# Kernel tuning notes

Hardware: AMD Instinct MI355X
Metric: run time of the kernel (lower is better)

## Reference

```python
import jax, jax.numpy as jnp
import numpy as np

HIDDEN = 384
NDIM = 3
N_POINTS = 100000
N_SUPER = 2048
MAX_DEG = 32
RADIUS = 0.045
INPUT_DIM = 3


def _sincos_embed(coords):
    # ContinuousSincosEmbed: dim=384, ndim=3 -> 128 channels per spatial dim (64 sin + 64 cos)
    eff = HIDDEN // NDIM  # 128
    omega = jnp.arange(0, eff, 2, dtype=jnp.float32) / eff
    freq = 1.0 / (10000.0 ** omega)  # [eff//2]
    out = coords[..., None] * freq  # [..., ndim, eff//2]
    emb = jnp.concatenate([jnp.sin(out), jnp.cos(out)], axis=-1)  # [..., ndim, eff]
    return emb.reshape(coords.shape[:-1] + (HIDDEN,))


def _radius_neighbors(pos, sn_idx):
    # numpy preprocessing equivalent of torch_geometric.nn.pool.radius with
    # max_num_neighbors=MAX_DEG; fixed-size padded [S, K] output + validity mask.
    nbr = np.zeros((N_SUPER, MAX_DEG), np.int32)
    mask = np.zeros((N_SUPER, MAX_DEG), bool)
    pos2 = (pos ** 2).sum(-1)
    r2 = RADIUS * RADIUS
    chunk = 128
    for i0 in range(0, N_SUPER, chunk):
        sp = pos[sn_idx[i0:i0 + chunk]]
        d2 = (sp ** 2).sum(-1)[:, None] + pos2[None, :] - 2.0 * (sp @ pos.T)
        within = d2 <= r2
        for j in range(sp.shape[0]):
            idx = np.nonzero(within[j])[0][:MAX_DEG]
            nbr[i0 + j, :len(idx)] = idx
            mask[i0 + j, :len(idx)] = True
    return nbr, mask


def setup_inputs() -> dict:
    rng = np.random.default_rng(0)
    pos = rng.random((N_POINTS, NDIM)).astype(np.float32)
    sn_idx = np.sort(rng.choice(N_POINTS, N_SUPER, replace=False)).astype(np.int32)
    nbr, mask = _radius_neighbors(pos, sn_idx)
    key = jax.random.key(0)
    ks = jax.random.split(key, 6)
    s = 0.02  # truncnormal002 init scale
    return {
        "input_pos": jnp.asarray(pos),
        "input_feat": jax.random.normal(ks[0], (N_POINTS, INPUT_DIM), jnp.float32),
        "supernode_idx": jnp.asarray(sn_idx),
        "neighbor_idx": jnp.asarray(nbr),
        "neighbor_mask": jnp.asarray(mask),
        "W_in": jax.random.normal(ks[1], (INPUT_DIM, HIDDEN), jnp.float32) * s,
        "b_in": jnp.zeros((HIDDEN,), jnp.float32),
        "W1": jax.random.normal(ks[2], (2 * HIDDEN, HIDDEN), jnp.float32) * s,
        "b1": jnp.zeros((HIDDEN,), jnp.float32),
        "W2": jax.random.normal(ks[3], (HIDDEN, HIDDEN), jnp.float32) * s,
        "b2": jnp.zeros((HIDDEN,), jnp.float32),
        "W_proj": jax.random.normal(ks[4], (2 * HIDDEN, HIDDEN), jnp.float32) * s,
        "b_proj": jnp.zeros((HIDDEN,), jnp.float32),
    }


def reference(input_pos, input_feat, supernode_idx, neighbor_idx, neighbor_mask,
              W_in, b_in, W1, b1, W2, b2, W_proj, b_proj):
    # point embeddings: continuous sincos pos embed + input feature projection
    x = _sincos_embed(input_pos) + input_feat @ W_in + b_in          # [N, D]
    sn = x[supernode_idx]                                            # [S, D] supernode pos embed
    src = x[neighbor_idx]                                            # [S, K, D] gathered neighbors
    dst = jnp.broadcast_to(sn[:, None, :], src.shape)                # [S, K, D]
    h = jnp.concatenate([src, dst], axis=-1)                         # [S, K, 2D]
    # message MLP (Linear -> GELU(exact) -> Linear), as nn.GELU default
    h = jax.nn.gelu(h @ W1 + b1, approximate=False) @ W2 + b2        # [S, K, D]
    # masked mean == segment_csr(..., reduce='mean') over variable-degree edges
    m = neighbor_mask[..., None].astype(h.dtype)
    agg = (h * m).sum(axis=1) / jnp.maximum(m.sum(axis=1), 1.0)      # [S, D]
    # readd_supernode_pos: concat supernode pos embed, project 2D -> D
    out = jnp.concatenate([agg, sn], axis=-1) @ W_proj + b_proj      # [S, D]
    return out[None]                                                 # [1, S, D] (batch_size=1)
```

## Files before the change

kernel.cpp:

```cpp
#include <hip/hip_runtime.h>
#include <hip/hip_bf16.h>
#include <cstdint>

#define HIDDEN 384
#define NSUPER 2048
#define MAXDEG 32
#define FRAGS (12*24*64)
#define WBLK  (FRAGS*8)

typedef __attribute__((ext_vector_type(8))) short bf16x8;
typedef __attribute__((ext_vector_type(4))) float f32x4;

__device__ inline unsigned short f2bf(float f) {
    unsigned int u = __float_as_uint(f);
    return (unsigned short)((u + 0x7fffu + ((u >> 16) & 1u)) >> 16);
}
__device__ inline float b2f(unsigned short s) {
    return __uint_as_float(((unsigned int)s) << 16);
}
__device__ inline bf16x8 pack8(const float* v) {
    union { bf16x8 v8; unsigned short u[8]; } u;
    #pragma unroll
    for (int i = 0; i < 8; ++i) u.u[i] = f2bf(v[i]);
    return u.v8;
}
__device__ inline float gelu(float y) {
    const float y2 = y * y;
    const float m  = __expf(y * fmaf(-0.0713548163f, y2, -1.5957691216f));
    return y * (1.0f / (1.0f + m));
}

__global__ __launch_bounds__(256)
void prep(const float* __restrict__ W1, const float* __restrict__ W2,
          const float* __restrict__ Wp, const unsigned int* __restrict__ mask,
          const float* __restrict__ pos, const float* __restrict__ feat,
          const int* __restrict__ sn_idx,
          const float* __restrict__ W_in, const float* __restrict__ b_in,
          unsigned short* __restrict__ w1sf, unsigned short* __restrict__ w1df,
          unsigned short* __restrict__ w2f,  unsigned short* __restrict__ wpf,
          unsigned short* __restrict__ snxb, int* __restrict__ flag) {
    const int b = blockIdx.x;
    const int t = threadIdx.x;
    if (b == 360) {
        __shared__ int s;
        if (t == 0) s = 0;
        __syncthreads();
        int bad = 0;
        for (int i = t; i < 16384; i += 256)
            if (mask[i] > 1u) bad = 1;
        if (bad) s = 1;
        __syncthreads();
        if (t == 0) *flag = s;
        return;
    }
    if (b > 360) {
        __shared__ float W4[HIDDEN][4];
        __shared__ float P6[64][7];
        const int eb = b - 361;
        if (t < 64) {
            const int pi = sn_idx[eb*64 + t];
            P6[t][0]=pos[pi*3];  P6[t][1]=pos[pi*3+1];  P6[t][2]=pos[pi*3+2];
            P6[t][3]=feat[pi*3]; P6[t][4]=feat[pi*3+1]; P6[t][5]=feat[pi*3+2];
        }
        for (int d = t; d < HIDDEN; d += 256) {
            W4[d][0]=W_in[d]; W4[d][1]=W_in[HIDDEN+d];
            W4[d][2]=W_in[2*HIDDEN+d]; W4[d][3]=b_in[d];
        }
        __syncthreads();
        const int er = t >> 2, seg = t & 3;
        float frA[8], frB[8];
        #pragma unroll
        for (int i = 0; i < 8; ++i) {
            frA[i] = exp2f(-(float)(seg*8 + i)      * 0.2076205059304601f);
            frB[i] = exp2f(-(float)(32 + seg*8 + i) * 0.2076205059304601f);
        }
        const float f0 = P6[er][3], f1 = P6[er][4], f2 = P6[er][5];
        #pragma unroll
        for (int cc = 0; cc < 3; ++cc) {
            const float pc = P6[er][cc];
            float sL[8], sH[8], cL[8], cH[8];
            #pragma unroll
            for (int i = 0; i < 8; ++i) {
                const float aL = pc*frA[i], aH = pc*frB[i];
                sL[i]=__sinf(aL); sH[i]=__sinf(aH); cL[i]=__cosf(aL); cH[i]=__cosf(aH);
            }
            #pragma unroll
            for (int q = 0; q < 4; ++q) {
                const float* bb = (q==0)?sL:(q==1)?sH:(q==2)?cL:cH;
                const int blk = cc*4 + q;
                float v[8];
                #pragma unroll
                for (int i = 0; i < 8; ++i) {
                    const int dim = blk*32 + seg*8 + i;
                    const float4 wv = *(const float4*)W4[dim];
                    v[i] = fmaf(f0, wv.x, fmaf(f1, wv.y, fmaf(f2, wv.z, bb[i] + wv.w)));
                }
                *(bf16x8*)&snxb[(size_t)(eb*64 + er)*HIDDEN + blk*32 + seg*8] = pack8(v);
            }
        }
        return;
    }
    const int grp = b / 72, sub = b % 72;
    const float* W; unsigned short* out;
    switch (grp) {
        case 0: W = W1;              out = w1sf; break;
        case 1: W = W1 + 384*HIDDEN; out = w1df; break;
        case 2: W = W2;              out = w2f;  break;
        case 3: W = Wp;              out = wpf;  break;
        default:W = Wp + 384*HIDDEN; out = wpf + WBLK; break;
    }
    const int idx = sub * 256 + t;
    const int l   = idx & 63;
    const int frag= idx >> 6;
    const int nt  = frag % 24;
    const int kt  = frag / 24;
    const int col = nt * 16 + (l & 15);
    const int k0  = kt * 32 + (l >> 4) * 8;
    unsigned int pk[4];
    #pragma unroll
    for (int j = 0; j < 4; ++j) {
        unsigned int lo = f2bf(W[(k0 + 2*j)     * HIDDEN + col]);
        unsigned int hi = f2bf(W[(k0 + 2*j + 1) * HIDDEN + col]);
        pk[j] = lo | (hi << 16);
    }
    *reinterpret_cast<uint4*>(&out[(size_t)idx * 8]) =
        *reinterpret_cast<const uint4*>(pk);
}

__global__ __launch_bounds__(256, 2)
void k_mlp(const float* __restrict__ pos, const float* __restrict__ feat,
           const int* __restrict__ nbr_idx, const void* __restrict__ mask_raw,
           const int* __restrict__ mask_fmt,
           const float* __restrict__ W_in, const float* __restrict__ b_in,
           const unsigned short* __restrict__ snxb,
           const unsigned short* __restrict__ W1sf,
           const unsigned short* __restrict__ W1df,
           const unsigned short* __restrict__ W2f,
           const float* __restrict__ b1, const float* __restrict__ b2,
           unsigned short* __restrict__ aggb)
{
    __shared__ unsigned short G[4*12*64*8];
    __shared__ ushort4 WINTB[HIDDEN];
    __shared__ float PF[64][7];
    __shared__ float CNT[2];

    const int t  = threadIdx.x;
    const int bm = blockIdx.x;
    const int l = t & 63, ng = t >> 6, lg = l >> 4, l15 = l & 15;

    bf16x8 bA[6], bB[6];
    #define LOADB(dst, Wf, kt)                                                  \
        { const unsigned short* bp_ = &Wf[((size_t)((kt)*24 + ng*6)*64 + l)*8]; \
          _Pragma("unroll")                                                     \
          for (int nt_ = 0; nt_ < 6; ++nt_)                                     \
              dst[nt_] = *(const bf16x8*)(bp_ + (size_t)nt_*512); }
    #define AREAD(a_, kt)                                                       \
        { _Pragma("unroll")                                                     \
          for (int mt_ = 0; mt_ < 4; ++mt_)                                     \
              a_[mt_] = *(const bf16x8*)&G[(size_t)(((mt_*12 + (kt))*64) + l)*8]; }
    #define MFMA6(bfr, a_)                                                      \
        { __builtin_amdgcn_s_setprio(1);                                        \
          _Pragma("unroll")                                                     \
          for (int mt_ = 0; mt_ < 4; ++mt_)                                     \
              _Pragma("unroll")                                                 \
              for (int nt_ = 0; nt_ < 6; ++nt_)                                 \
                  acc[mt_][nt_] = __builtin_amdgcn_mfma_f32_16x16x32_bf16(      \
                      a_[mt_], bfr[nt_], acc[mt_][nt_], 0, 0, 0);               \
          __builtin_amdgcn_s_setprio(0); }

    if (t < 64) {
        const int e  = bm*64 + t;
        const int pi = nbr_idx[e];
        PF[t][0]=pos[pi*3];  PF[t][1]=pos[pi*3+1];  PF[t][2]=pos[pi*3+2];
        PF[t][3]=feat[pi*3]; PF[t][4]=feat[pi*3+1]; PF[t][5]=feat[pi*3+2];
        const int fmt = *mask_fmt;
        const int mv  = fmt ? (int)((const unsigned char*)mask_raw)[e]
                            : ((const int*)mask_raw)[e];
        PF[t][6] = mv ? 1.0f : 0.0f;
    }
    for (int d = t; d < HIDDEN; d += 256) {
        ushort4 wv;
        wv.x = f2bf(W_in[d]); wv.y = f2bf(W_in[HIDDEN+d]);
        wv.z = f2bf(W_in[2*HIDDEN+d]); wv.w = f2bf(b_in[d]);
        WINTB[d] = wv;
    }
    float b1r[6];
    #pragma unroll
    for (int nt = 0; nt < 6; ++nt) b1r[nt] = b1[ng*96 + nt*16 + l15];
    __syncthreads();
    if (t < 2) {
        float c = 0.f;
        for (int s = 0; s < 32; ++s) c += PF[t*32+s][6];
        CNT[t] = c;
    }

    const int er = t >> 2, seg = t & 3;
    float frA[8], frB[8];
    #pragma unroll
    for (int i = 0; i < 8; ++i) {
        frA[i] = exp2f(-(float)(seg*8 + i)      * 0.2076205059304601f);
        frB[i] = exp2f(-(float)(32 + seg*8 + i) * 0.2076205059304601f);
    }
    const float f0 = PF[er][3], f1 = PF[er][4], f2 = PF[er][5];
    const float pc0 = PF[er][0], pc1 = PF[er][1], pc2 = PF[er][2];
    const int slotbase = (er>>4)*12*64 + seg*16 + (er&15);

    #define EMB(kt_)                                                            \
        { const float pc = ((kt_)>>2)==0 ? pc0 : (((kt_)>>2)==1 ? pc1 : pc2);   \
          float v[8];                                                           \
          _Pragma("unroll")                                                     \
          for (int i = 0; i < 8; ++i) {                                         \
              const float fr = ((kt_)&1) ? frB[i] : frA[i];                     \
              const float aa = pc * fr;                                         \
              const float base = (((kt_)>>1)&1) ? __cosf(aa) : __sinf(aa);      \
              const ushort4 wv = WINTB[(kt_)*32 + seg*8 + i];                   \
              v[i] = fmaf(f0, b2f(wv.x), fmaf(f1, b2f(wv.y),                    \
                     fmaf(f2, b2f(wv.z), base + b2f(wv.w))));                   \
          }                                                                     \
          *(bf16x8*)&G[(size_t)(slotbase + (kt_)*64)*8] = pack8(v); }

    f32x4 acc[4][6];
    #pragma unroll
    for (int mt=0; mt<4; ++mt)
        #pragma unroll
        for (int nt=0; nt<6; ++nt) acc[mt][nt] = (f32x4){0.f,0.f,0.f,0.f};

    const unsigned short* snx0 = &snxb[(size_t)(bm*2 + 0)*HIDDEN];
    const unsigned short* snx1 = &snxb[(size_t)(bm*2 + 1)*HIDDEN];
    #pragma unroll
    for (int kt = 0; kt < 12; ++kt) {
        LOADB(bA, W1df, kt);
        bf16x8 s0 = *(const bf16x8*)&snx0[kt*32 + lg*8];
        bf16x8 s1 = *(const bf16x8*)&snx1[kt*32 + lg*8];
        EMB(kt);
        __builtin_amdgcn_s_setprio(1);
        #pragma unroll
        for (int nt = 0; nt < 6; ++nt) {
            acc[0][nt] = __builtin_amdgcn_mfma_f32_16x16x32_bf16(s0, bA[nt], acc[0][nt], 0,0,0);
            acc[1][nt] = __builtin_amdgcn_mfma_f32_16x16x32_bf16(s0, bA[nt], acc[1][nt], 0,0,0);
            acc[2][nt] = __builtin_amdgcn_mfma_f32_16x16x32_bf16(s1, bA[nt], acc[2][nt], 0,0,0);
            acc[3][nt] = __builtin_amdgcn_mfma_f32_16x16x32_bf16(s1, bA[nt], acc[3][nt], 0,0,0);
        }
        __builtin_amdgcn_s_setprio(0);
    }
    __syncthreads();

    LOADB(bA, W1sf, 0); LOADB(bB, W1sf, 1);
    #pragma unroll
    for (int kt = 0; kt < 12; kt += 2) {
        bf16x8 a[4];
        AREAD(a, kt);
        MFMA6(bA, a);
        if (kt + 2 < 12) LOADB(bA, W1sf, kt + 2);
        AREAD(a, kt + 1);
        MFMA6(bB, a);
        if (kt + 3 < 12) LOADB(bB, W1sf, kt + 3);
    }
    __syncthreads();

    #pragma unroll
    for (int mt=0; mt<4; ++mt) {
        #pragma unroll
        for (int nt=0; nt<6; ++nt) {
            const int col = ng*96 + nt*16 + l15;
            const float bb1 = b1r[nt];
            const int base = ((mt*12 + (col>>5))*64 + ((col>>3)&3)*16 + lg*4)*8 + (col&7);
            #pragma unroll
            for (int r=0; r<4; ++r)
                G[base + r*8] = f2bf(gelu(acc[mt][nt][r] + bb1));
        }
    }
    __syncthreads();

    #pragma unroll
    for (int mt=0; mt<4; ++mt)
        #pragma unroll
        for (int nt=0; nt<6; ++nt) acc[mt][nt] = (f32x4){0.f,0.f,0.f,0.f};
    LOADB(bA, W2f, 0); LOADB(bB, W2f, 1);
    #pragma unroll
    for (int kt = 0; kt < 12; kt += 2) {
        bf16x8 a[4];
        AREAD(a, kt);
        MFMA6(bA, a);
        if (kt + 2 < 12) LOADB(bA, W2f, kt + 2);
        AREAD(a, kt + 1);
        MFMA6(bB, a);
        if (kt + 3 < 12) LOADB(bB, W2f, kt + 3);
    }

    #pragma unroll
    for (int nt=0; nt<6; ++nt) {
        const int col = ng*96 + nt*16 + l15;
        float s0 = 0.f, s1 = 0.f;
        #pragma unroll
        for (int mt=0; mt<4; ++mt) {
            float p = 0.f;
            #pragma unroll
            for (int r=0; r<4; ++r)
                p += PF[mt*16 + lg*4 + r][6] * acc[mt][nt][r];
            if (mt < 2) s0 += p; else s1 += p;
        }
        s0 += __shfl_xor(s0,16); s0 += __shfl_xor(s0,32);
        s1 += __shfl_xor(s1,16); s1 += __shfl_xor(s1,32);
        if (lg == 0) {
            const float bb = b2[col];
            const int sn0 = bm*2;
            const float c0 = CNT[0], c1 = CNT[1];
            aggb[(size_t)sn0*HIDDEN + col]     = f2bf(s0 / fmaxf(c0,1.f) + bb*(c0>0.f?1.f:0.f));
            aggb[(size_t)(sn0+1)*HIDDEN + col] = f2bf(s1 / fmaxf(c1,1.f) + bb*(c1>0.f?1.f:0.f));
        }
    }
    #undef LOADB
    #undef AREAD
    #undef MFMA6
    #undef EMB
}

__global__ __launch_bounds__(256)
void k_proj(const unsigned short* __restrict__ aggb,
            const unsigned short* __restrict__ snxb,
            const unsigned short* __restrict__ wpf,
            const float* __restrict__ bp, float* __restrict__ out) {
    const int rg = blockIdx.x >> 2, cq = blockIdx.x & 3;
    const int t = threadIdx.x, w = t>>6, l = t&63, lg = l>>4, l15 = l&15;
    const int wgm = w>>1, wgn = w&1;
    const int r0 = rg*64 + wgm*32;
    const int ntb = cq*6 + wgn*3;
    f32x4 acc[2][3];
    #pragma unroll
    for (int mt=0; mt<2; ++mt)
        #pragma unroll
        for (int nt=0; nt<3; ++nt) acc[mt][nt] = (f32x4){0.f,0.f,0.f,0.f};
    #pragma unroll 2
    for (int kt = 0; kt < 24; ++kt) {
        const unsigned short* Ab = (kt < 12) ? aggb : snxb;
        const unsigned short* Wb = (kt < 12) ? wpf  : wpf + WBLK;
        const int ktt = (kt < 12) ? kt : kt - 12;
        bf16x8 a[2], bfr[3];
        const unsigned short* bpp = &Wb[((size_t)(ktt*24 + ntb)*64 + l)*8];
        #pragma unroll
        for (int nt=0; nt<3; ++nt) bfr[nt] = *(const bf16x8*)(bpp + (size_t)nt*512);
        #pragma unroll
        for (int mt=0; mt<2; ++mt)
            a[mt] = *(const bf16x8*)&Ab[(size_t)(r0 + mt*16 + l15)*HIDDEN + ktt*32 + lg*8];
        #pragma unroll
        for (int mt=0; mt<2; ++mt)
            #pragma unroll
            for (int nt=0; nt<3; ++nt)
                acc[mt][nt] = __builtin_amdgcn_mfma_f32_16x16x32_bf16(a[mt], bfr[nt], acc[mt][nt], 0,0,0);
    }
    #pragma unroll
    for (int mt=0; mt<2; ++mt)
        #pragma unroll
        for (int nt=0; nt<3; ++nt) {
            const int col = cq*96 + wgn*48 + nt*16 + l15;
            #pragma unroll
            for (int r=0; r<4; ++r) {
                const int row = r0 + mt*16 + lg*4 + r;
                out[(size_t)row*HIDDEN + col] = acc[mt][nt][r] + bp[col];
            }
        }
}

extern "C" void kernel_launch(void* const* d_in, const int* in_sizes, int n_in,
                              void* d_out, int out_size, void* d_ws, size_t ws_size,
                              hipStream_t stream) {
    const float* pos   = (const float*)d_in[0];
    const float* feat  = (const float*)d_in[1];
    const int*   sn    = (const int*)d_in[2];
    const int*   nbr   = (const int*)d_in[3];
    const void*  mask  = d_in[4];
    const float* W_in  = (const float*)d_in[5];
    const float* b_in  = (const float*)d_in[6];
    const float* W1    = (const float*)d_in[7];
    const float* b1    = (const float*)d_in[8];
    const float* W2    = (const float*)d_in[9];
    const float* b2    = (const float*)d_in[10];
    const float* Wp    = (const float*)d_in[11];
    const float* bpv   = (const float*)d_in[12];
    float* out = (float*)d_out;

    char* base = (char*)d_ws;
    int* flag = (int*)base;
    unsigned short* w1sf = (unsigned short*)(base + 256);
    unsigned short* w1df = w1sf + WBLK;
    unsigned short* w2f  = w1df + WBLK;
    unsigned short* wpf  = w2f  + WBLK;
    unsigned short* snxb = wpf  + 2*(size_t)WBLK;
    unsigned short* aggb = snxb + (size_t)NSUPER*HIDDEN;

    hipLaunchKernelGGL(prep, dim3(393), dim3(256), 0, stream,
                       W1, W2, Wp, (const unsigned int*)mask,
                       pos, feat, sn, W_in, b_in,
                       w1sf, w1df, w2f, wpf, snxb, flag);
    hipLaunchKernelGGL(k_mlp, dim3(1024), dim3(256), 0, stream,
                       pos, feat, nbr, mask, flag, W_in, b_in,
                       snxb, w1sf, w1df, w2f, b1, b2, aggb);
    hipLaunchKernelGGL(k_proj, dim3(128), dim3(256), 0, stream,
                       aggb, snxb, wpf, bpv, out);
}
```

Baseline: 84.44 us.

## Move second MLP linear after masked mean aggregation into separate GEMM kernel

The second linear layer is linear, so the masked mean of its output equals the masked mean of the GELU activations multiplied by W2, plus the bias when the node has neighbors. k_mlp now only computes GEMM1 plus GELU and reduces over neighbors, writing pre-aggregated bf16 rows and counts. A new k_agg kernel applies W2 and the bias on the 2048 supernode rows. This removes the per-edge W2 GEMM and the LDS staging of activations, at the cost of an extra launch and an extra workspace buffer.

```diff
diff --git a/kernel.cpp b/kernel.cpp
--- a/kernel.cpp
+++ b/kernel.cpp
@@ -135,9 +135,8 @@
            const unsigned short* __restrict__ snxb,
            const unsigned short* __restrict__ W1sf,
            const unsigned short* __restrict__ W1df,
-           const unsigned short* __restrict__ W2f,
-           const float* __restrict__ b1, const float* __restrict__ b2,
-           unsigned short* __restrict__ aggb)
+           const float* __restrict__ b1,
+           unsigned short* __restrict__ aggpre, float* __restrict__ cntf)
 {
     __shared__ unsigned short G[4*12*64*8];
     __shared__ ushort4 WINTB[HIDDEN];
@@ -256,64 +255,78 @@
         MFMA6(bB, a);
         if (kt + 3 < 12) LOADB(bB, W1sf, kt + 3);
     }
-    __syncthreads();
-
-    #pragma unroll
-    for (int mt=0; mt<4; ++mt) {
-        #pragma unroll
-        for (int nt=0; nt<6; ++nt) {
-            const int col = ng*96 + nt*16 + l15;
-            const float bb1 = b1r[nt];
-            const int base = ((mt*12 + (col>>5))*64 + ((col>>3)&3)*16 + lg*4)*8 + (col&7);
-            #pragma unroll
-            for (int r=0; r<4; ++r)
-                G[base + r*8] = f2bf(gelu(acc[mt][nt][r] + bb1));
-        }
-    }
-    __syncthreads();
-
-    #pragma unroll
-    for (int mt=0; mt<4; ++mt)
-        #pragma unroll
-        for (int nt=0; nt<6; ++nt) acc[mt][nt] = (f32x4){0.f,0.f,0.f,0.f};
-    LOADB(bA, W2f, 0); LOADB(bB, W2f, 1);
-    #pragma unroll
-    for (int kt = 0; kt < 12; kt += 2) {
-        bf16x8 a[4];
-        AREAD(a, kt);
-        MFMA6(bA, a);
-        if (kt + 2 < 12) LOADB(bA, W2f, kt + 2);
-        AREAD(a, kt + 1);
-        MFMA6(bB, a);
-        if (kt + 3 < 12) LOADB(bB, W2f, kt + 3);
-    }
 
     #pragma unroll
     for (int nt=0; nt<6; ++nt) {
         const int col = ng*96 + nt*16 + l15;
+        const float bb1 = b1r[nt];
         float s0 = 0.f, s1 = 0.f;
         #pragma unroll
         for (int mt=0; mt<4; ++mt) {
             float p = 0.f;
             #pragma unroll
             for (int r=0; r<4; ++r)
-                p += PF[mt*16 + lg*4 + r][6] * acc[mt][nt][r];
+                p += PF[mt*16 + lg*4 + r][6] * gelu(acc[mt][nt][r] + bb1);
             if (mt < 2) s0 += p; else s1 += p;
         }
         s0 += __shfl_xor(s0,16); s0 += __shfl_xor(s0,32);
         s1 += __shfl_xor(s1,16); s1 += __shfl_xor(s1,32);
         if (lg == 0) {
-            const float bb = b2[col];
             const int sn0 = bm*2;
-            const float c0 = CNT[0], c1 = CNT[1];
-            aggb[(size_t)sn0*HIDDEN + col]     = f2bf(s0 / fmaxf(c0,1.f) + bb*(c0>0.f?1.f:0.f));
-            aggb[(size_t)(sn0+1)*HIDDEN + col] = f2bf(s1 / fmaxf(c1,1.f) + bb*(c1>0.f?1.f:0.f));
-        }
-    }
+            aggpre[(size_t)sn0*HIDDEN + col]     = f2bf(s0 / fmaxf(CNT[0],1.f));
+            aggpre[(size_t)(sn0+1)*HIDDEN + col] = f2bf(s1 / fmaxf(CNT[1],1.f));
+        }
+    }
+    if (t < 2) cntf[bm*2 + t] = CNT[t];
     #undef LOADB
     #undef AREAD
     #undef MFMA6
     #undef EMB
+}
+
+__global__ __launch_bounds__(256)
+void k_agg(const unsigned short* __restrict__ aggpre,
+           const unsigned short* __restrict__ w2f,
+           const float* __restrict__ b2, const float* __restrict__ cntf,
+           unsigned short* __restrict__ aggb) {
+    const int rg = blockIdx.x >> 2, cq = blockIdx.x & 3;
+    const int t = threadIdx.x, w = t>>6, l = t&63, lg = l>>4, l15 = l&15;
+    const int wgm = w>>1, wgn = w&1;
+    const int r0 = rg*64 + wgm*32;
+    const int ntb = cq*6 + wgn*3;
+    f32x4 acc[2][3];
+    #pragma unroll
+    for (int mt=0; mt<2; ++mt)
+        #pragma unroll
+        for (int nt=0; nt<3; ++nt) acc[mt][nt] = (f32x4){0.f,0.f,0.f,0.f};
+    #pragma unroll 2
+    for (int kt = 0; kt < 12; ++kt) {
+        bf16x8 a[2], bfr[3];
+        const unsigned short* bpp = &w2f[((size_t)(kt*24 + ntb)*64 + l)*8];
+        #pragma unroll
+        for (int nt=0; nt<3; ++nt) bfr[nt] = *(const bf16x8*)(bpp + (size_t)nt*512);
+        #pragma unroll
+        for (int mt=0; mt<2; ++mt)
+            a[mt] = *(const bf16x8*)&aggpre[(size_t)(r0 + mt*16 + l15)*HIDDEN + kt*32 + lg*8];
+        #pragma unroll
+        for (int mt=0; mt<2; ++mt)
+            #pragma unroll
+            for (int nt=0; nt<3; ++nt)
+                acc[mt][nt] = __builtin_amdgcn_mfma_f32_16x16x32_bf16(a[mt], bfr[nt], acc[mt][nt], 0,0,0);
+    }
+    #pragma unroll
+    for (int mt=0; mt<2; ++mt)
+        #pragma unroll
+        for (int nt=0; nt<3; ++nt) {
+            const int col = cq*96 + wgn*48 + nt*16 + l15;
+            const float bb = b2[col];
+            #pragma unroll
+            for (int r=0; r<4; ++r) {
+                const int row = r0 + mt*16 + lg*4 + r;
+                const float nz = (cntf[row] > 0.f) ? 1.f : 0.f;
+                aggb[(size_t)row*HIDDEN + col] = f2bf(acc[mt][nt][r] + bb*nz);
+            }
+        }
 }
 
 __global__ __launch_bounds__(256)
@@ -388,6 +401,8 @@
     unsigned short* wpf  = w2f  + WBLK;
     unsigned short* snxb = wpf  + 2*(size_t)WBLK;
     unsigned short* aggb = snxb + (size_t)NSUPER*HIDDEN;
+    unsigned short* aggp = aggb + (size_t)NSUPER*HIDDEN;
+    float* cntf = (float*)(aggp + (size_t)NSUPER*HIDDEN);
 
     hipLaunchKernelGGL(prep, dim3(393), dim3(256), 0, stream,
                        W1, W2, Wp, (const unsigned int*)mask,
@@ -395,7 +410,9 @@
                        w1sf, w1df, w2f, wpf, snxb, flag);
     hipLaunchKernelGGL(k_mlp, dim3(1024), dim3(256), 0, stream,
                        pos, feat, nbr, mask, flag, W_in, b_in,
-                       snxb, w1sf, w1df, w2f, b1, b2, aggb);
+                       snxb, w1sf, w1df, b1, aggp, cntf);
+    hipLaunchKernelGGL(k_agg, dim3(128), dim3(256), 0, stream,
+                       aggp, w2f, b2, cntf, aggb);
     hipLaunchKernelGGL(k_proj, dim3(128), dim3(256), 0, stream,
                        aggb, snxb, wpf, bpv, out);
 }
```

Measured after the change: 81.17 us. -3.9%, faster.

## Fold W2 into projection via linearity and split embedding into separate kernel

Applied to the files above, without the earlier changes.

Because the masked mean is linear, the second MLP layer is pushed past the aggregation: W2·Wp is precomputed in prep (fp32 matmul per fragment) and b2·Wp is added conditioned on nonzero count. This removes the whole 64x384x384 second GEMM per block in k_mlp. The neighbor embedding is moved to a separate k_emb kernel that writes MFMA-ready fragments to global workspace, chunked to fit ws_size, and k_mlp now reads A-fragments from global instead of LDS. The trade-off is a costly naive W2·Wp product in prep on every call, extra global traffic for embeddings, and a rounding change from the fused bf16 weight.

```diff
diff --git a/kernel.cpp b/kernel.cpp
--- a/kernel.cpp
+++ b/kernel.cpp
@@ -4,9 +4,9 @@
 
 #define HIDDEN 384
 #define NSUPER 2048
-#define MAXDEG 32
 #define FRAGS (12*24*64)
 #define WBLK  (FRAGS*8)
+#define EGSLOTS 3072
 
 typedef __attribute__((ext_vector_type(8))) short bf16x8;
 typedef __attribute__((ext_vector_type(4))) float f32x4;
@@ -14,9 +14,6 @@
 __device__ inline unsigned short f2bf(float f) {
     unsigned int u = __float_as_uint(f);
     return (unsigned short)((u + 0x7fffu + ((u >> 16) & 1u)) >> 16);
-}
-__device__ inline float b2f(unsigned short s) {
-    return __uint_as_float(((unsigned int)s) << 16);
 }
 __device__ inline bf16x8 pack8(const float* v) {
     union { bf16x8 v8; unsigned short u[8]; } u;
@@ -32,16 +29,18 @@
 
 __global__ __launch_bounds__(256)
 void prep(const float* __restrict__ W1, const float* __restrict__ W2,
-          const float* __restrict__ Wp, const unsigned int* __restrict__ mask,
+          const float* __restrict__ Wp, const float* __restrict__ b2,
+          const unsigned int* __restrict__ mask,
           const float* __restrict__ pos, const float* __restrict__ feat,
           const int* __restrict__ sn_idx,
           const float* __restrict__ W_in, const float* __restrict__ b_in,
           unsigned short* __restrict__ w1sf, unsigned short* __restrict__ w1df,
-          unsigned short* __restrict__ w2f,  unsigned short* __restrict__ wpf,
+          unsigned short* __restrict__ w2pf, unsigned short* __restrict__ wpbf,
+          float* __restrict__ c2p,
           unsigned short* __restrict__ snxb, int* __restrict__ flag) {
     const int b = blockIdx.x;
     const int t = threadIdx.x;
-    if (b == 360) {
+    if (b == 288) {
         __shared__ int s;
         if (t == 0) s = 0;
         __syncthreads();
@@ -53,10 +52,19 @@
         if (t == 0) *flag = s;
         return;
     }
-    if (b > 360) {
+    if (b == 289) {
+        for (int col = t; col < HIDDEN; col += 256) {
+            float s = 0.f;
+            for (int k = 0; k < HIDDEN; ++k)
+                s += b2[k] * Wp[(size_t)k*HIDDEN + col];
+            c2p[col] = s;
+        }
+        return;
+    }
+    if (b >= 290) {
         __shared__ float W4[HIDDEN][4];
         __shared__ float P6[64][7];
-        const int eb = b - 361;
+        const int eb = b - 290;
         if (t < 64) {
             const int pi = sn_idx[eb*64 + t];
             P6[t][0]=pos[pi*3];  P6[t][1]=pos[pi*3+1];  P6[t][2]=pos[pi*3+2];
@@ -100,14 +108,40 @@
         }
         return;
     }
+    if (b >= 216) {
+        const int idx = (b - 216)*256 + t;
+        const int l = idx & 63, frag = idx >> 6;
+        const int nt = frag % 24, kt = frag / 24;
+        const int col = nt*16 + (l & 15);
+        const int r0  = kt*32 + (l >> 4)*8;
+        float a8[8];
+        #pragma unroll
+        for (int j = 0; j < 8; ++j) a8[j] = 0.f;
+        for (int k = 0; k < HIDDEN; k += 4) {
+            const float wp0 = Wp[(size_t)(k+0)*HIDDEN + col];
+            const float wp1 = Wp[(size_t)(k+1)*HIDDEN + col];
+            const float wp2 = Wp[(size_t)(k+2)*HIDDEN + col];
+            const float wp3 = Wp[(size_t)(k+3)*HIDDEN + col];
+            #pragma unroll
+            for (int j = 0; j < 8; ++j) {
+                const float4 w2v = *(const float4*)&W2[(size_t)(r0+j)*HIDDEN + k];
+                a8[j] += w2v.x*wp0 + w2v.y*wp1 + w2v.z*wp2 + w2v.w*wp3;
+            }
+        }
+        unsigned int pk[4];
+        #pragma unroll
+        for (int j = 0; j < 4; ++j)
+            pk[j] = (unsigned int)f2bf(a8[2*j]) | ((unsigned int)f2bf(a8[2*j+1]) << 16);
+        *reinterpret_cast<uint4*>(&w2pf[(size_t)idx*8]) =
+            *reinterpret_cast<const uint4*>(pk);
+        return;
+    }
     const int grp = b / 72, sub = b % 72;
     const float* W; unsigned short* out;
     switch (grp) {
         case 0: W = W1;              out = w1sf; break;
         case 1: W = W1 + 384*HIDDEN; out = w1df; break;
-        case 2: W = W2;              out = w2f;  break;
-        case 3: W = Wp;              out = wpf;  break;
-        default:W = Wp + 384*HIDDEN; out = wpf + WBLK; break;
+        default:W = Wp + 384*HIDDEN; out = wpbf; break;
     }
     const int idx = sub * 256 + t;
     const int l   = idx & 63;
@@ -119,34 +153,104 @@
     unsigned int pk[4];
     #pragma unroll
     for (int j = 0; j < 4; ++j) {
-        unsigned int lo = f2bf(W[(k0 + 2*j)     * HIDDEN + col]);
-        unsigned int hi = f2bf(W[(k0 + 2*j + 1) * HIDDEN + col]);
+        unsigned int lo = f2bf(W[(size_t)(k0 + 2*j)     * HIDDEN + col]);
+        unsigned int hi = f2bf(W[(size_t)(k0 + 2*j + 1) * HIDDEN + col]);
         pk[j] = lo | (hi << 16);
     }
     *reinterpret_cast<uint4*>(&out[(size_t)idx * 8]) =
         *reinterpret_cast<const uint4*>(pk);
 }
 
+__global__ __launch_bounds__(256)
+void k_emb(const float* __restrict__ pos, const float* __restrict__ feat,
+           const int* __restrict__ nbr_idx,
+           const float* __restrict__ W_in, const float* __restrict__ b_in,
+           unsigned short* __restrict__ eG, int cbase)
+{
+    __shared__ float PF[64][6];
+    __shared__ float W4[HIDDEN][4];
+    const int t = threadIdx.x;
+    const int bmL = blockIdx.x, bmG = cbase + bmL;
+    if (t < 64) {
+        const int pi = nbr_idx[bmG*64 + t];
+        PF[t][0]=pos[pi*3];  PF[t][1]=pos[pi*3+1];  PF[t][2]=pos[pi*3+2];
+        PF[t][3]=feat[pi*3]; PF[t][4]=feat[pi*3+1]; PF[t][5]=feat[pi*3+2];
+    }
+    for (int d = t; d < HIDDEN; d += 256) {
+        W4[d][0]=W_in[d]; W4[d][1]=W_in[HIDDEN+d];
+        W4[d][2]=W_in[2*HIDDEN+d]; W4[d][3]=b_in[d];
+    }
+    __syncthreads();
+    const int er = t >> 2, seg = t & 3;
+    float frA[8], frB[8];
+    #pragma unroll
+    for (int i = 0; i < 8; ++i) {
+        frA[i] = exp2f(-(float)(seg*8 + i)      * 0.2076205059304601f);
+        frB[i] = exp2f(-(float)(32 + seg*8 + i) * 0.2076205059304601f);
+    }
+    const float f0 = PF[er][3], f1 = PF[er][4], f2 = PF[er][5];
+    const int slotb = (er>>4)*768 + seg*16 + (er&15);
+    unsigned short* dst = &eG[(size_t)bmL * EGSLOTS * 8];
+    #pragma unroll
+    for (int cc = 0; cc < 3; ++cc) {
+        const float pc = PF[er][cc];
+        float sL[8], sH[8], cL[8], cH[8];
+        #pragma unroll
+        for (int i = 0; i < 8; ++i) {
+            const float aL = pc*frA[i], aH = pc*frB[i];
+            sL[i]=__sinf(aL); sH[i]=__sinf(aH); cL[i]=__cosf(aL); cH[i]=__cosf(aH);
+        }
+        #pragma unroll
+        for (int q = 0; q < 4; ++q) {
+            const float* bb = (q==0)?sL:(q==1)?sH:(q==2)?cL:cH;
+            const int blk = cc*4 + q;
+            float v[8];
+            #pragma unroll
+            for (int i = 0; i < 8; ++i) {
+                const int dim = blk*32 + seg*8 + i;
+                const float4 wv = *(const float4*)W4[dim];
+                v[i] = fmaf(f0, wv.x, fmaf(f1, wv.y, fmaf(f2, wv.z, bb[i] + wv.w)));
+            }
+            *(bf16x8*)&dst[(size_t)(slotb + blk*64)*8] = pack8(v);
+        }
+    }
+}
+
 __global__ __launch_bounds__(256, 2)
-void k_mlp(const float* __restrict__ pos, const float* __restrict__ feat,
-           const int* __restrict__ nbr_idx, const void* __restrict__ mask_raw,
+void k_mlp(const int* __restrict__ nbr_idx, const void* __restrict__ mask_raw,
            const int* __restrict__ mask_fmt,
-           const float* __restrict__ W_in, const float* __restrict__ b_in,
            const unsigned short* __restrict__ snxb,
            const unsigned short* __restrict__ W1sf,
            const unsigned short* __restrict__ W1df,
-           const unsigned short* __restrict__ W2f,
-           const float* __restrict__ b1, const float* __restrict__ b2,
-           unsigned short* __restrict__ aggb)
+           const unsigned short* __restrict__ eG,
+           const float* __restrict__ b1,
+           unsigned short* __restrict__ aggpre, float* __restrict__ cntf,
+           int cbase)
 {
-    __shared__ unsigned short G[4*12*64*8];
-    __shared__ ushort4 WINTB[HIDDEN];
-    __shared__ float PF[64][7];
+    __shared__ float MV[64];
     __shared__ float CNT[2];
-
-    const int t  = threadIdx.x;
-    const int bm = blockIdx.x;
+    const int t = threadIdx.x;
+    const int bmL = blockIdx.x, bmG = cbase + bmL;
     const int l = t & 63, ng = t >> 6, lg = l >> 4, l15 = l & 15;
+
+    if (t < 64) {
+        const int e = bmG*64 + t;
+        const int fmt = *mask_fmt;
+        const int mv = fmt ? (int)((const unsigned char*)mask_raw)[e]
+                           : ((const int*)mask_raw)[e];
+        MV[t] = mv ? 1.0f : 0.0f;
+    }
+    __syncthreads();
+    if (t < 2) {
+        float c = 0.f;
+        for (int s = 0; s < 32; ++s) c += MV[t*32+s];
+        CNT[t] = c;
+    }
+    __syncthreads();
+
+    float b1r[6];
+    #pragma unroll
+    for (int nt = 0; nt < 6; ++nt) b1r[nt] = b1[ng*96 + nt*16 + l15];
 
     bf16x8 bA[6], bB[6];
     #define LOADB(dst, Wf, kt)                                                  \
@@ -154,10 +258,10 @@
           _Pragma("unroll")                                                     \
           for (int nt_ = 0; nt_ < 6; ++nt_)                                     \
               dst[nt_] = *(const bf16x8*)(bp_ + (size_t)nt_*512); }
-    #define AREAD(a_, kt)                                                       \
+    #define ALOAD(a_, kt)                                                       \
         { _Pragma("unroll")                                                     \
           for (int mt_ = 0; mt_ < 4; ++mt_)                                     \
-              a_[mt_] = *(const bf16x8*)&G[(size_t)(((mt_*12 + (kt))*64) + l)*8]; }
+              a_[mt_] = *(const bf16x8*)&eGb[(size_t)(((mt_*12 + (kt))*64) + l)*8]; }
     #define MFMA6(bfr, a_)                                                      \
         { __builtin_amdgcn_s_setprio(1);                                        \
           _Pragma("unroll")                                                     \
@@ -168,71 +272,24 @@
                       a_[mt_], bfr[nt_], acc[mt_][nt_], 0, 0, 0);               \
           __builtin_amdgcn_s_setprio(0); }
 
-    if (t < 64) {
-        const int e  = bm*64 + t;
-        const int pi = nbr_idx[e];
-        PF[t][0]=pos[pi*3];  PF[t][1]=pos[pi*3+1];  PF[t][2]=pos[pi*3+2];
-        PF[t][3]=feat[pi*3]; PF[t][4]=feat[pi*3+1]; PF[t][5]=feat[pi*3+2];
-        const int fmt = *mask_fmt;
-        const int mv  = fmt ? (int)((const unsigned char*)mask_raw)[e]
-                            : ((const int*)mask_raw)[e];
-        PF[t][6] = mv ? 1.0f : 0.0f;
-    }
-    for (int d = t; d < HIDDEN; d += 256) {
-        ushort4 wv;
-        wv.x = f2bf(W_in[d]); wv.y = f2bf(W_in[HIDDEN+d]);
-        wv.z = f2bf(W_in[2*HIDDEN+d]); wv.w = f2bf(b_in[d]);
-        WINTB[d] = wv;
-    }
-    float b1r[6];
-    #pragma unroll
-    for (int nt = 0; nt < 6; ++nt) b1r[nt] = b1[ng*96 + nt*16 + l15];
-    __syncthreads();
-    if (t < 2) {
-        float c = 0.f;
-        for (int s = 0; s < 32; ++s) c += PF[t*32+s][6];
-        CNT[t] = c;
-    }
-
-    const int er = t >> 2, seg = t & 3;
-    float frA[8], frB[8];
-    #pragma unroll
-    for (int i = 0; i < 8; ++i) {
-        frA[i] = exp2f(-(float)(seg*8 + i)      * 0.2076205059304601f);
-        frB[i] = exp2f(-(float)(32 + seg*8 + i) * 0.2076205059304601f);
-    }
-    const float f0 = PF[er][3], f1 = PF[er][4], f2 = PF[er][5];
-    const float pc0 = PF[er][0], pc1 = PF[er][1], pc2 = PF[er][2];
-    const int slotbase = (er>>4)*12*64 + seg*16 + (er&15);
-
-    #define EMB(kt_)                                                            \
-        { const float pc = ((kt_)>>2)==0 ? pc0 : (((kt_)>>2)==1 ? pc1 : pc2);   \
-          float v[8];                                                           \
-          _Pragma("unroll")                                                     \
-          for (int i = 0; i < 8; ++i) {                                         \
-              const float fr = ((kt_)&1) ? frB[i] : frA[i];                     \
-              const float aa = pc * fr;                                         \
-              const float base = (((kt_)>>1)&1) ? __cosf(aa) : __sinf(aa);      \
-              const ushort4 wv = WINTB[(kt_)*32 + seg*8 + i];                   \
-              v[i] = fmaf(f0, b2f(wv.x), fmaf(f1, b2f(wv.y),                    \
-                     fmaf(f2, b2f(wv.z), base + b2f(wv.w))));                   \
-          }                                                                     \
-          *(bf16x8*)&G[(size_t)(slotbase + (kt_)*64)*8] = pack8(v); }
-
     f32x4 acc[4][6];
     #pragma unroll
     for (int mt=0; mt<4; ++mt)
         #pragma unroll
         for (int nt=0; nt<6; ++nt) acc[mt][nt] = (f32x4){0.f,0.f,0.f,0.f};
 
-    const unsigned short* snx0 = &snxb[(size_t)(bm*2 + 0)*HIDDEN];
-    const unsigned short* snx1 = &snxb[(size_t)(bm*2 + 1)*HIDDEN];
+    const unsigned short* eGb = &eG[(size_t)bmL * EGSLOTS * 8];
+
+    bf16x8 aX[4], aY[4];
+    ALOAD(aX, 0);
+    ALOAD(aY, 1);
+    const unsigned short* snx0 = &snxb[(size_t)(bmG*2 + 0)*HIDDEN];
+    const unsigned short* snx1 = &snxb[(size_t)(bmG*2 + 1)*HIDDEN];
     #pragma unroll
     for (int kt = 0; kt < 12; ++kt) {
         LOADB(bA, W1df, kt);
         bf16x8 s0 = *(const bf16x8*)&snx0[kt*32 + lg*8];
         bf16x8 s1 = *(const bf16x8*)&snx1[kt*32 + lg*8];
-        EMB(kt);
         __builtin_amdgcn_s_setprio(1);
         #pragma unroll
         for (int nt = 0; nt < 6; ++nt) {
@@ -243,84 +300,57 @@
         }
         __builtin_amdgcn_s_setprio(0);
     }
-    __syncthreads();
-
-    LOADB(bA, W1sf, 0); LOADB(bB, W1sf, 1);
+
+    LOADB(bA, W1sf, 0);
+    LOADB(bB, W1sf, 1);
     #pragma unroll
     for (int kt = 0; kt < 12; kt += 2) {
-        bf16x8 a[4];
-        AREAD(a, kt);
-        MFMA6(bA, a);
-        if (kt + 2 < 12) LOADB(bA, W1sf, kt + 2);
-        AREAD(a, kt + 1);
-        MFMA6(bB, a);
-        if (kt + 3 < 12) LOADB(bB, W1sf, kt + 3);
-    }
-    __syncthreads();
-
-    #pragma unroll
-    for (int mt=0; mt<4; ++mt) {
-        #pragma unroll
-        for (int nt=0; nt<6; ++nt) {
-            const int col = ng*96 + nt*16 + l15;
-            const float bb1 = b1r[nt];
-            const int base = ((mt*12 + (col>>5))*64 + ((col>>3)&3)*16 + lg*4)*8 + (col&7);
-            #pragma unroll
-            for (int r=0; r<4; ++r)
-                G[base + r*8] = f2bf(gelu(acc[mt][nt][r] + bb1));
-        }
-    }
-    __syncthreads();
-
+        MFMA6(bA, aX);
+        if (kt + 2 < 12) { ALOAD(aX, kt + 2); LOADB(bA, W1sf, kt + 2); }
+        MFMA6(bB, aY);
+        if (kt + 3 < 12) { ALOAD(aY, kt + 3); LOADB(bB, W1sf, kt + 3); }
+    }
+
+    float mvr[4][4];
     #pragma unroll
     for (int mt=0; mt<4; ++mt)
         #pragma unroll
-        for (int nt=0; nt<6; ++nt) acc[mt][nt] = (f32x4){0.f,0.f,0.f,0.f};
-    LOADB(bA, W2f, 0); LOADB(bB, W2f, 1);
-    #pragma unroll
-    for (int kt = 0; kt < 12; kt += 2) {
-        bf16x8 a[4];
-        AREAD(a, kt);
-        MFMA6(bA, a);
-        if (kt + 2 < 12) LOADB(bA, W2f, kt + 2);
-        AREAD(a, kt + 1);
-        MFMA6(bB, a);
-        if (kt + 3 < 12) LOADB(bB, W2f, kt + 3);
-    }
-
+        for (int r=0; r<4; ++r)
+            mvr[mt][r] = MV[mt*16 + lg*4 + r];
     #pragma unroll
     for (int nt=0; nt<6; ++nt) {
         const int col = ng*96 + nt*16 + l15;
+        const float bb1 = b1r[nt];
         float s0 = 0.f, s1 = 0.f;
         #pragma unroll
         for (int mt=0; mt<4; ++mt) {
             float p = 0.f;
             #pragma unroll
             for (int r=0; r<4; ++r)
-                p += PF[mt*16 + lg*4 + r][6] * acc[mt][nt][r];
+                p += mvr[mt][r] * gelu(acc[mt][nt][r] + bb1);
             if (mt < 2) s0 += p; else s1 += p;
         }
         s0 += __shfl_xor(s0,16); s0 += __shfl_xor(s0,32);
         s1 += __shfl_xor(s1,16); s1 += __shfl_xor(s1,32);
         if (lg == 0) {
-            const float bb = b2[col];
-            const int sn0 = bm*2;
-            const float c0 = CNT[0], c1 = CNT[1];
-            aggb[(size_t)sn0*HIDDEN + col]     = f2bf(s0 / fmaxf(c0,1.f) + bb*(c0>0.f?1.f:0.f));
-            aggb[(size_t)(sn0+1)*HIDDEN + col] = f2bf(s1 / fmaxf(c1,1.f) + bb*(c1>0.f?1.f:0.f));
-        }
-    }
+            const int sn0 = bmG*2;
+            aggpre[(size_t)sn0*HIDDEN + col]     = f2bf(s0 / fmaxf(CNT[0],1.f));
+            aggpre[(size_t)(sn0+1)*HIDDEN + col] = f2bf(s1 / fmaxf(CNT[1],1.f));
+        }
+    }
+    if (t < 2) cntf[bmG*2 + t] = CNT[t];
     #undef LOADB
-    #undef AREAD
+    #undef ALOAD
     #undef MFMA6
-    #undef EMB
 }
 
 __global__ __launch_bounds__(256)
-void k_proj(const unsigned short* __restrict__ aggb,
+void k_proj(const unsigned short* __restrict__ aggp,
             const unsigned short* __restrict__ snxb,
-            const unsigned short* __restrict__ wpf,
-            const float* __restrict__ bp, float* __restrict__ out) {
+            const unsigned short* __restrict__ w2pf,
+            const unsigned short* __restrict__ wpbf,
+            const float* __restrict__ bp, const float* __restrict__ c2p,
+            const float* __restrict__ cntf, float* __restrict__ out) {
     const int rg = blockIdx.x >> 2, cq = blockIdx.x & 3;
     const int t = threadIdx.x, w = t>>6, l = t&63, lg = l>>4, l15 = l&15;
     const int wgm = w>>1, wgn = w&1;
@@ -333,8 +363,8 @@
         for (int nt=0; nt<3; ++nt) acc[mt][nt] = (f32x4){0.f,0.f,0.f,0.f};
     #pragma unroll 2
     for (int kt = 0; kt < 24; ++kt) {
-        const unsigned short* Ab = (kt < 12) ? aggb : snxb;
-        const unsigned short* Wb = (kt < 12) ? wpf  : wpf + WBLK;
+        const unsigned short* Ab = (kt < 12) ? aggp : snxb;
+        const unsigned short* Wb = (kt < 12) ? w2pf : wpbf;
         const int ktt = (kt < 12) ? kt : kt - 12;
         bf16x8 a[2], bfr[3];
         const unsigned short* bpp = &Wb[((size_t)(ktt*24 + ntb)*64 + l)*8];
@@ -354,10 +384,13 @@
         #pragma unroll
         for (int nt=0; nt<3; ++nt) {
             const int col = cq*96 + wgn*48 + nt*16 + l15;
+            const float bbp = bp[col];
+            const float cc2 = c2p[col];
             #pragma unroll
             for (int r=0; r<4; ++r) {
                 const int row = r0 + mt*16 + lg*4 + r;
-                out[(size_t)row*HIDDEN + col] = acc[mt][nt][r] + bp[col];
+                const float nz = (cntf[row] > 0.f) ? 1.f : 0.f;
+                out[(size_t)row*HIDDEN + col] = acc[mt][nt][r] + bbp + nz*cc2;
             }
         }
 }
@@ -381,21 +414,34 @@
     float* out = (float*)d_out;
 
     char* base = (char*)d_ws;
-    int* flag = (int*)base;
-    unsigned short* w1sf = (unsigned short*)(base + 256);
+    int*   flag = (int*)base;
+    float* c2p  = (float*)(base + 256);
+    unsigned short* w1sf = (unsigned short*)(base + 2048);
     unsigned short* w1df = w1sf + WBLK;
-    unsigned short* w2f  = w1df + WBLK;
-    unsigned short* wpf  = w2f  + WBLK;
-    unsigned short* snxb = wpf  + 2*(size_t)WBLK;
-    unsigned short* aggb = snxb + (size_t)NSUPER*HIDDEN;
-
-    hipLaunchKernelGGL(prep, dim3(393), dim3(256), 0, stream,
-                       W1, W2, Wp, (const unsigned int*)mask,
+    unsigned short* w2pf = w1df + WBLK;
+    unsigned short* wpbf = w2pf + WBLK;
+    unsigned short* snxb = wpbf + WBLK;
+    unsigned short* aggp = snxb + (size_t)NSUPER*HIDDEN;
+    float* cntf = (float*)(aggp + (size_t)NSUPER*HIDDEN);
+    unsigned short* eG = (unsigned short*)((char*)cntf + NSUPER*sizeof(float));
+    const size_t base_need = (size_t)((char*)eG - base);
+    const size_t EG_BYTES = (size_t)65536 * HIDDEN * 2;
+
+    int C = 1;
+    while (C < 16 && base_need + EG_BYTES / (size_t)C > ws_size) C <<= 1;
+    const int bpc = 1024 / C;
+
+    hipLaunchKernelGGL(prep, dim3(322), dim3(256), 0, stream,
+                       W1, W2, Wp, b2, (const unsigned int*)mask,
                        pos, feat, sn, W_in, b_in,
-                       w1sf, w1df, w2f, wpf, snxb, flag);
-    hipLaunchKernelGGL(k_mlp, dim3(1024), dim3(256), 0, stream,
-                       pos, feat, nbr, mask, flag, W_in, b_in,
-                       snxb, w1sf, w1df, w2f, b1, b2, aggb);
+                       w1sf, w1df, w2pf, wpbf, c2p, snxb, flag);
+    for (int c = 0; c < C; ++c) {
+        hipLaunchKernelGGL(k_emb, dim3(bpc), dim3(256), 0, stream,
+                           pos, feat, nbr, W_in, b_in, eG, c*bpc);
+        hipLaunchKernelGGL(k_mlp, dim3(bpc), dim3(256), 0, stream,
+                           nbr, mask, flag, snxb, w1sf, w1df, eG, b1,
+                           aggp, cntf, c*bpc);
+    }
     hipLaunchKernelGGL(k_proj, dim3(128), dim3(256), 0, stream,
-                       aggb, snxb, wpf, bpv, out);
-}
+                       aggp, snxb, w2pf, wpbf, bpv, c2p, cntf, out);
+}
```

New measurement: 113.4 us. +34.3%, slower.
